# Optimization experiments

Hardware: AMD Instinct MI355X
Metric: run time of the kernel (lower is better)

The kernel has to match this reference:

```python
import jax, jax.numpy as jnp
import numpy as np
import math

B, S, D = 2, 2048, 768
H, KS, VS = 12, 64, 64
MAX_DIST, NUM_BASES, MIN_HALF_LIFE = 1000, 16, 3.0


def _exponential_basis_features():
    # positions -max_dist..max_dist, exponential basis as in RelativePositionalBias
    positions = np.arange(-MAX_DIST, MAX_DIST + 1)
    abs_pos = np.abs(positions).astype(np.float32)
    max_range = math.log2(MAX_DIST)
    half_lives = np.power(2.0, np.linspace(MIN_HALF_LIFE, max_range, NUM_BASES)).reshape(1, -1)
    feats = np.exp(-math.log(2.0) * abs_pos[:, None] / half_lives)  # [2*max_dist+1, num_bases]
    return jnp.asarray(feats, dtype=jnp.float32)


def setup_inputs() -> dict:
    key = jax.random.key(0)
    ks = jax.random.split(key, 6)
    x = jax.random.normal(ks[0], (B, S, D), dtype=jnp.float32)
    # torch nn.Linear weight convention: [out_features, in_features], applied as x @ W.T
    Wq = jax.random.normal(ks[1], (H * KS, D), dtype=jnp.float32) * 0.02
    Wk = jax.random.normal(ks[2], (H * KS, D), dtype=jnp.float32) * 0.02
    Wv = jax.random.normal(ks[3], (H * VS, D), dtype=jnp.float32) * 0.02
    # original zero-inits w_o; use small random for a non-degenerate correctness baseline
    Wo = jax.random.normal(ks[4], (D, H * VS), dtype=jnp.float32) * 0.02
    basis_weights = jax.random.normal(ks[5], (H, NUM_BASES), dtype=jnp.float32)
    basis_features = _exponential_basis_features()  # buffer (non-learned)
    return {"x": x, "Wq": Wq, "Wk": Wk, "Wv": Wv, "Wo": Wo,
            "basis_weights": basis_weights, "basis_features": basis_features}


def _relative_bias(basis_features, basis_weights, q_len, k_len):
    rel = jnp.arange(k_len)[None, :] - jnp.arange(q_len)[:, None]
    rel = jnp.clip(rel, -MAX_DIST, MAX_DIST) + MAX_DIST  # [q, k] indices
    basis = basis_features[rel]                          # [q, k, nb]
    return jnp.einsum('qkb,hb->hqk', basis, basis_weights)


def reference(x, Wq, Wk, Wv, Wo, basis_weights, basis_features):
    b, s, _ = x.shape
    q = (x @ Wq.T).reshape(b, s, H, KS)
    k = (x @ Wk.T).reshape(b, s, H, KS)
    v = (x @ Wv.T).reshape(b, s, H, VS)
    scale = math.sqrt(KS)
    scores = jnp.einsum('bqhc,bkhc->bhqk', q, k) / scale
    scores = scores + _relative_bias(basis_features, basis_weights, s, s)[None]
    attn = jax.nn.softmax(scores, axis=-1)  # dropout is identity in eval
    out = jnp.einsum('bhqk,bkhv->bqhv', attn, v).reshape(b, s, H * VS)
    out = out @ Wo.T
    return out, attn
```

## Files before the change

kernel.cpp:

```cpp
#include <hip/hip_runtime.h>

typedef _Float16 f16;
typedef __attribute__((ext_vector_type(4))) _Float16 f16x4;
typedef __attribute__((ext_vector_type(8))) _Float16 f16x8;
typedef __attribute__((ext_vector_type(4))) float f32x4;
typedef __attribute__((ext_vector_type(16))) float f32x16;

#define B_ 2
#define S_ 2048
#define DMODEL 768
#define H_ 12
#define HS 64
#define NB_ 16
#define QKV_LD 2304

#define ZERO16 {0.f,0.f,0.f,0.f,0.f,0.f,0.f,0.f,0.f,0.f,0.f,0.f,0.f,0.f,0.f,0.f}

__device__ __forceinline__ void gload16(const f16* g, f16* lds) {
    __builtin_amdgcn_global_load_lds((const __attribute__((address_space(1))) void*)g,
                                     (__attribute__((address_space(3))) void*)lds, 16, 0, 0);
}
#define WAIT_VM0_BARRIER()  do { asm volatile("s_waitcnt vmcnt(0) lgkmcnt(0)" ::: "memory"); \
                                 __builtin_amdgcn_s_barrier(); } while (0)

__global__ __launch_bounds__(256) void prep_kernel(const float* __restrict__ x,
                                                   const float* __restrict__ Wq,
                                                   const float* __restrict__ Wk,
                                                   const float* __restrict__ Wv,
                                                   const float* __restrict__ Wo,
                                                   const float* __restrict__ bw,
                                                   const float* __restrict__ bf,
                                                   f16* __restrict__ xb,
                                                   f16* __restrict__ wqkv16,
                                                   f16* __restrict__ wo16,
                                                   float* __restrict__ biasTab) {
    int bid = blockIdx.x;
    int t = threadIdx.x;
    if (bid < 5376) {
        const float* src;
        f16* dst;
        float scale = 1.0f;
        int i;
        if (bid < 3072) {
            i = bid * 256 + t; src = x; dst = xb;
        } else if (bid < 4800) {
            i = (bid - 3072) * 256 + t;
            dst = wqkv16;
            if (i < 147456)      { src = Wq; scale = 0.18033688011112f; }
            else if (i < 294912) { src = Wk - 147456 * 4; }
            else                 { src = Wv - 294912 * 4; }
        } else {
            i = (bid - 4800) * 256 + t; src = Wo; dst = wo16;
        }
        f32x4 v = reinterpret_cast<const f32x4*>(src)[i];
        union { f16 h[4]; unsigned long long u; } o;
        o.h[0] = (f16)(v.x * scale);
        o.h[1] = (f16)(v.y * scale);
        o.h[2] = (f16)(v.z * scale);
        o.h[3] = (f16)(v.w * scale);
        reinterpret_cast<unsigned long long*>(dst)[i] = o.u;
    } else {
        int idx = (bid - 5376) * 256 + t;
        if (idx >= H_ * 4095) return;
        int h = idx / 4095, d = idx % 4095;
        int rel = min(1000, max(-1000, d - 2047));
        int r = rel + 1000;
        float s = 0.f;
#pragma unroll
        for (int tt = 0; tt < NB_; ++tt) s += bf[r * NB_ + tt] * bw[h * NB_ + tt];
        biasTab[h * 4095 + d] = s * 1.44269504088896f;
    }
}

__global__ __launch_bounds__(256) void vtrans_kernel(const f16* __restrict__ qkv,
                                                     f16* __restrict__ vt) {
    __shared__ f16 tile[64][72];
    int blk = blockIdx.x;
    int tb = blk & 31;
    int bh = blk >> 5;
    int b = bh / H_;
    int tok0 = tb << 6;
    int t = threadIdx.x;
    const f16* src = qkv + (size_t)b * S_ * QKV_LD + 1536 + (bh - b * H_) * 64;
#pragma unroll
    for (int j = 0; j < 2; ++j) {
        int u = t + (j << 8);
        int r = u >> 3, c = (u & 7) << 3;
        *reinterpret_cast<f16x8*>(&tile[r][c]) =
            *reinterpret_cast<const f16x8*>(src + (size_t)(tok0 + r) * QKV_LD + c);
    }
    __syncthreads();
    f16* dst = vt + (size_t)bh * 64 * S_ + tok0;
#pragma unroll
    for (int j = 0; j < 2; ++j) {
        int u = t + (j << 8);
        int v = u >> 3, tc = (u & 7) << 3;
        union { f16 h8[8]; f16x8 v8; } o;
#pragma unroll
        for (int i = 0; i < 8; ++i) o.h8[i] = tile[tc + i][v];
        *reinterpret_cast<f16x8*>(&dst[(size_t)v * S_ + tc]) = o.v8;
    }
}

template <typename OutT, int NT>
__global__ __launch_bounds__(256) void gemm_nt(const f16* __restrict__ A,
                                               const f16* __restrict__ Bm,
                                               OutT* __restrict__ C,
                                               int M, int N, int K, float alpha) {
    constexpr int NF  = NT / 32;
    constexpr int BCH = NT / 64;
    __shared__ __align__(16) f16 As[2][128 * 32];
    __shared__ __align__(16) f16 Bs[2][NT * 32];
    const int tiles_n = N / NT;
    int tm = blockIdx.x / tiles_n, tn = blockIdx.x % tiles_n;
    int m0 = tm << 7, n0 = tn * NT;
    int t = threadIdx.x;
    int w = t >> 6, l = t & 63;
    int wr = w >> 1, wc = w & 1;
    int fr = l & 15, hi = l >> 4;
    f32x4 acc[4][NF] = {};

#define GEMM_STAGE(buf, k0)                                                        \
    do {                                                                           \
        _Pragma("unroll")                                                          \
        for (int j = 0; j < 2; ++j) {                                              \
            int u = t + (j << 8);                                                  \
            int row = u >> 2, ch = u & 3;                                          \
            int gcol = (k0) + ((ch ^ (row & 3)) << 3);                             \
            gload16(&A[(size_t)(m0 + row) * K + gcol], As[buf] + (w << 9) + (j << 11)); \
        }                                                                          \
        _Pragma("unroll")                                                          \
        for (int j = 0; j < BCH; ++j) {                                            \
            int u = t + (j << 8);                                                  \
            int row = u >> 2, ch = u & 3;                                          \
            int gcol = (k0) + ((ch ^ (row & 3)) << 3);                             \
            gload16(&Bm[(size_t)(n0 + row) * K + gcol], Bs[buf] + (w << 9) + (j << 11)); \
        }                                                                          \
    } while (0)

    const int nk = K >> 5;
    GEMM_STAGE(0, 0);
    WAIT_VM0_BARRIER();
    for (int kt = 0; kt < nk; ++kt) {
        int buf = kt & 1;
        if (kt + 1 < nk) GEMM_STAGE(buf ^ 1, (kt + 1) << 5);
        f16x8 af[4], bfv[NF];
#pragma unroll
        for (int m = 0; m < 4; ++m) {
            int row = wr * 64 + m * 16 + fr;
            af[m] = *reinterpret_cast<const f16x8*>(&As[buf][row * 32 + ((hi ^ (fr & 3)) << 3)]);
        }
#pragma unroll
        for (int n = 0; n < NF; ++n) {
            int row = wc * (NT / 2) + n * 16 + fr;
            bfv[n] = *reinterpret_cast<const f16x8*>(&Bs[buf][row * 32 + ((hi ^ (fr & 3)) << 3)]);
        }
#pragma unroll
        for (int m = 0; m < 4; ++m)
#pragma unroll
            for (int n = 0; n < NF; ++n)
                acc[m][n] = __builtin_amdgcn_mfma_f32_16x16x32_f16(af[m], bfv[n], acc[m][n], 0, 0, 0);
        WAIT_VM0_BARRIER();
    }
#undef GEMM_STAGE
    int cc = l & 15, cr = (l >> 4) << 2;
#pragma unroll
    for (int m = 0; m < 4; ++m)
#pragma unroll
        for (int n = 0; n < NF; ++n)
#pragma unroll
            for (int j = 0; j < 4; ++j) {
                int rg = m0 + wr * 64 + m * 16 + cr + j;
                int cg = n0 + wc * (NT / 2) + n * 16 + cc;
                C[(size_t)rg * N + cg] = (OutT)(acc[m][n][j] * alpha);
            }
}

#define PSWZ(row) ((((row) >> 2) & 3) << 3)
__global__ __launch_bounds__(256, 3) void attn_kernel(const f16* __restrict__ qp,
                                                      const f16* __restrict__ kp,
                                                      const f16* __restrict__ vt,
                                                      const float* __restrict__ biasTab,
                                                      float* __restrict__ attn_out,
                                                      f16* __restrict__ ctx_out) {
    __shared__ __align__(16) union {
        f16 ks1[2][128 * 64];
        struct { f16 ks[2][64 * 64]; f16 vs[2][64 * 64]; } p2;
    } ar;
    __shared__ __align__(16) f16 psh[64][72];
    __shared__ float bias_l[2112];
    __shared__ float red_l[64][2];
    __shared__ float li_s[64];

    int orig = blockIdx.x;
    int blk = (orig & 7) * 96 + (orig >> 3);
    int qt = blk & 31;
    int bh = blk >> 5;
    int h = bh % H_;
    int b = bh / H_;
    int q0 = qt << 6;

    int t = threadIdx.x;
    int w = t >> 6, l = t & 63;
    int wq = w >> 1, wk = w & 1;
    int col = l & 31;
    int hi = l >> 5;
    int hi4 = hi << 2, hi8 = hi << 3;

    const size_t rowbase = (size_t)b * S_ * QKV_LD + (size_t)h * HS;
    const f16* vbase = vt + (size_t)bh * HS * S_;

    f16x8 qf[4];
    {
        const f16* qrow = qp + rowbase + (size_t)(q0 + wq * 32 + col) * QKV_LD + hi8;
#pragma unroll
        for (int ci = 0; ci < 4; ++ci) qf[ci] = *reinterpret_cast<const f16x8*>(qrow + ci * 16);
    }

    {
        const float* bt = biasTab + h * 4095 + (1984 - q0);
        for (int i = t; i < 2111; i += 256) bias_l[i] = bt[i];
    }

#define P1_STAGE(buf, kb0)                                                          \
    do {                                                                            \
        _Pragma("unroll")                                                           \
        for (int j = 0; j < 4; ++j) {                                               \
            int u = t + (j << 8);                                                   \
            int row = u >> 3, ch = u & 7;                                           \
            gload16(kp + rowbase + (size_t)((kb0) + row) * QKV_LD + ((ch ^ (row & 7)) << 3), \
                    ar.ks1[buf] + (w << 9) + (j << 11));                            \
        }                                                                           \
    } while (0)

    float lsum[16];
#pragma unroll
    for (int r = 0; r < 16; ++r) lsum[r] = 0.f;

    P1_STAGE(0, 0);
    WAIT_VM0_BARRIER();
    for (int jt = 0; jt < 16; ++jt) {
        int buf = jt & 1;
        if (jt + 1 < 16) P1_STAGE(buf ^ 1, (jt + 1) << 7);
#pragma unroll
        for (int half = 0; half < 2; ++half) {
            int krow = half * 64 + wk * 32 + col;
            f32x16 s = ZERO16;
#pragma unroll
            for (int ci = 0; ci < 4; ++ci) {
                f16x8 kf = *reinterpret_cast<const f16x8*>(
                    &ar.ks1[buf][krow * 64 + (((ci * 2 + hi) ^ (krow & 7)) << 3)]);
                s = __builtin_amdgcn_mfma_f32_32x32x16_f16(qf[ci], kf, s, 0, 0, 0);
            }
            int kcol = (jt << 7) + krow;
            const float* bl = bias_l + (kcol + 63 - (wq * 32 + hi4));
#pragma unroll
            for (int r = 0; r < 16; ++r) {
                const int cr = (r & 3) + 8 * (r >> 2);
                lsum[r] += __builtin_amdgcn_exp2f(s[r] + bl[-cr]);
            }
        }
        WAIT_VM0_BARRIER();
    }
#undef P1_STAGE

#pragma unroll
    for (int off = 1; off < 32; off <<= 1) {
#pragma unroll
        for (int r = 0; r < 16; ++r) lsum[r] += __shfl_xor(lsum[r], off);
    }
    if (col == 0) {
#pragma unroll
        for (int r = 0; r < 16; ++r)
            red_l[wq * 32 + (r & 3) + 8 * (r >> 2) + hi4][wk] = lsum[r];
    }
    __syncthreads();
    if (t < 64) li_s[t] = 1.0f / (red_l[t][0] + red_l[t][1]);
    __syncthreads();
    float lreg[16];
#pragma unroll
    for (int r = 0; r < 16; ++r) lreg[r] = li_s[wq * 32 + (r & 3) + 8 * (r >> 2) + hi4];

#define P2_STAGE(buf, kb0)                                                          \
    do {                                                                            \
        _Pragma("unroll")                                                           \
        for (int j = 0; j < 2; ++j) {                                               \
            int u = t + (j << 8);                                                   \
            int row = u >> 3, ch = u & 7;                                           \
            int sw = ((ch ^ (row & 7)) << 3);                                       \
            gload16(kp + rowbase + (size_t)((kb0) + row) * QKV_LD + sw,             \
                    ar.p2.ks[buf] + (w << 9) + (j << 11));                          \
            gload16(vbase + (size_t)row * S_ + (kb0) + sw,                          \
                    ar.p2.vs[buf] + (w << 9) + (j << 11));                          \
        }                                                                           \
    } while (0)

    f32x16 oacc = ZERO16;
    float* aout = attn_out + (((size_t)b * H_ + h) * S_ + q0) * S_;
    const int kcol_loc = wk * 32 + col;

    P2_STAGE(0, 0);
    WAIT_VM0_BARRIER();
    float pstash[16];
    for (int tix = 0; tix < 32; ++tix) {
        int buf = tix & 1;
        int kb0 = tix << 6;
        if (tix + 1 < 32) P2_STAGE(buf ^ 1, kb0 + 64);
        __builtin_amdgcn_sched_barrier(0);
        f32x16 s = ZERO16;
#pragma unroll
        for (int ci = 0; ci < 4; ++ci) {
            f16x8 kf = *reinterpret_cast<const f16x8*>(
                &ar.p2.ks[buf][kcol_loc * 64 + (((ci * 2 + hi) ^ (kcol_loc & 7)) << 3)]);
            s = __builtin_amdgcn_mfma_f32_32x32x16_f16(qf[ci], kf, s, 0, 0, 0);
        }
        int kcol = kb0 + kcol_loc;
        const float* bl = bias_l + (kcol + 63 - (wq * 32 + hi4));
#pragma unroll
        for (int r = 0; r < 16; ++r) {
            const int cr = (r & 3) + 8 * (r >> 2);
            int row = wq * 32 + cr + hi4;
            float p = __builtin_amdgcn_exp2f(s[r] + bl[-cr]) * lreg[r];
            pstash[r] = p;
            psh[row][kcol_loc ^ PSWZ(row)] = (f16)p;
        }
        asm volatile("s_waitcnt lgkmcnt(0)" ::: "memory");
        __builtin_amdgcn_s_barrier();
        __builtin_amdgcn_sched_barrier(0);
        {
            const int rowq = wq * 32 + col;
            const int sw = PSWZ(rowq);
#pragma unroll
            for (int ci = 0; ci < 4; ++ci) {
                f16x8 pa = *reinterpret_cast<const f16x8*>(&psh[rowq][(ci * 16 + hi8) ^ sw]);
                f16x8 vf = *reinterpret_cast<const f16x8*>(
                    &ar.p2.vs[buf][kcol_loc * 64 + (((ci * 2 + hi) ^ (kcol_loc & 7)) << 3)]);
                oacc = __builtin_amdgcn_mfma_f32_32x32x16_f16(pa, vf, oacc, 0, 0, 0);
            }
        }
        asm volatile("s_waitcnt vmcnt(0)" ::: "memory");
        __builtin_amdgcn_s_barrier();
#pragma unroll
        for (int r = 0; r < 16; ++r) {
            const int cr = (r & 3) + 8 * (r >> 2);
            int row = wq * 32 + cr + hi4;
            __builtin_nontemporal_store(pstash[r], &aout[(size_t)row * S_ + kcol]);
        }
    }
#undef P2_STAGE

    {
        f16* cbase = ctx_out + ((size_t)b * S_ + q0) * DMODEL + h * HS + kcol_loc;
#pragma unroll
        for (int r = 0; r < 16; ++r) {
            int row = wq * 32 + (r & 3) + 8 * (r >> 2) + hi4;
            cbase[(size_t)row * DMODEL] = (f16)oacc[r];
        }
    }
}

extern "C" void kernel_launch(void* const* d_in, const int* in_sizes, int n_in,
                              void* d_out, int out_size, void* d_ws, size_t ws_size,
                              hipStream_t stream) {
    const float* x     = (const float*)d_in[0];
    const float* Wq    = (const float*)d_in[1];
    const float* Wk    = (const float*)d_in[2];
    const float* Wv    = (const float*)d_in[3];
    const float* Wo    = (const float*)d_in[4];
    const float* bw    = (const float*)d_in[5];
    const float* bfeat = (const float*)d_in[6];

    char* ws = (char*)d_ws;
    f16*   xb      = (f16*)(ws + 0);
    f16*   vt      = (f16*)(ws + 0);
    f16*   qkv     = (f16*)(ws + 6291456);
    f16*   ctx     = (f16*)(ws + 25165824);
    f16*   wqkv16  = (f16*)(ws + 31457280);
    f16*   wo16    = (f16*)(ws + 34996224);
    float* biasTab = (float*)(ws + 36175872);

    float* out0 = (float*)d_out;
    float* attn = out0 + (size_t)B_ * S_ * DMODEL;

    prep_kernel<<<5568, 256, 0, stream>>>(x, Wq, Wk, Wv, Wo, bw, bfeat,
                                          xb, wqkv16, wo16, biasTab);

    gemm_nt<f16, 128><<<32 * 18, 256, 0, stream>>>(xb, wqkv16, qkv, 4096, QKV_LD, 768, 1.0f);

    vtrans_kernel<<<768, 256, 0, stream>>>(qkv, vt);

    attn_kernel<<<B_ * H_ * (S_ / 64), 256, 0, stream>>>(
        qkv + 0, qkv + 768, vt, biasTab, attn, ctx);

    gemm_nt<float, 64><<<32 * 12, 256, 0, stream>>>(ctx, wo16, out0, 4096, DMODEL, 768, 1.0f);
}
```

Baseline: 171.8 us.

## Split attention into separate row-sum and output kernels for higher occupancy

Splits the fused two-pass attention kernel into two launches. The first kernel computes softmax row sums using 64-row K tiles and smaller LDS, with launch bounds allowing 5 blocks per CU, and writes the inverse sums to workspace. The second kernel reloads Q, bias and the inverse sums, then computes probabilities, the attn output and the context as before. The aim is better latency hiding in the sum pass, at the cost of an extra launch, a second load of Q and bias, and a workspace buffer that reuses the wqkv16 region after the QKV GEMM is done with it.

```diff
diff --git a/kernel.cpp b/kernel.cpp
--- a/kernel.cpp
+++ b/kernel.cpp
@@ -176,21 +176,13 @@
             }
 }
 
-#define PSWZ(row) ((((row) >> 2) & 3) << 3)
-__global__ __launch_bounds__(256, 3) void attn_kernel(const f16* __restrict__ qp,
-                                                      const f16* __restrict__ kp,
-                                                      const f16* __restrict__ vt,
-                                                      const float* __restrict__ biasTab,
-                                                      float* __restrict__ attn_out,
-                                                      f16* __restrict__ ctx_out) {
-    __shared__ __align__(16) union {
-        f16 ks1[2][128 * 64];
-        struct { f16 ks[2][64 * 64]; f16 vs[2][64 * 64]; } p2;
-    } ar;
-    __shared__ __align__(16) f16 psh[64][72];
+__global__ __launch_bounds__(256, 5) void attn_pass1(const f16* __restrict__ qp,
+                                                     const f16* __restrict__ kp,
+                                                     const float* __restrict__ biasTab,
+                                                     float* __restrict__ linv_g) {
+    __shared__ __align__(16) f16 ks[2][64 * 64];
     __shared__ float bias_l[2112];
     __shared__ float red_l[64][2];
-    __shared__ float li_s[64];
 
     int orig = blockIdx.x;
     int blk = (orig & 7) * 96 + (orig >> 3);
@@ -208,7 +200,6 @@
     int hi4 = hi << 2, hi8 = hi << 3;
 
     const size_t rowbase = (size_t)b * S_ * QKV_LD + (size_t)h * HS;
-    const f16* vbase = vt + (size_t)bh * HS * S_;
 
     f16x8 qf[4];
     {
@@ -216,7 +207,6 @@
 #pragma unroll
         for (int ci = 0; ci < 4; ++ci) qf[ci] = *reinterpret_cast<const f16x8*>(qrow + ci * 16);
     }
-
     {
         const float* bt = biasTab + h * 4095 + (1984 - q0);
         for (int i = t; i < 2111; i += 256) bias_l[i] = bt[i];
@@ -225,11 +215,11 @@
 #define P1_STAGE(buf, kb0)                                                          \
     do {                                                                            \
         _Pragma("unroll")                                                           \
-        for (int j = 0; j < 4; ++j) {                                               \
+        for (int j = 0; j < 2; ++j) {                                               \
             int u = t + (j << 8);                                                   \
             int row = u >> 3, ch = u & 7;                                           \
             gload16(kp + rowbase + (size_t)((kb0) + row) * QKV_LD + ((ch ^ (row & 7)) << 3), \
-                    ar.ks1[buf] + (w << 9) + (j << 11));                            \
+                    ks[buf] + (w << 9) + (j << 11));                                \
         }                                                                           \
     } while (0)
 
@@ -239,26 +229,23 @@
 
     P1_STAGE(0, 0);
     WAIT_VM0_BARRIER();
-    for (int jt = 0; jt < 16; ++jt) {
-        int buf = jt & 1;
-        if (jt + 1 < 16) P1_STAGE(buf ^ 1, (jt + 1) << 7);
-#pragma unroll
-        for (int half = 0; half < 2; ++half) {
-            int krow = half * 64 + wk * 32 + col;
-            f32x16 s = ZERO16;
-#pragma unroll
-            for (int ci = 0; ci < 4; ++ci) {
-                f16x8 kf = *reinterpret_cast<const f16x8*>(
-                    &ar.ks1[buf][krow * 64 + (((ci * 2 + hi) ^ (krow & 7)) << 3)]);
-                s = __builtin_amdgcn_mfma_f32_32x32x16_f16(qf[ci], kf, s, 0, 0, 0);
-            }
-            int kcol = (jt << 7) + krow;
-            const float* bl = bias_l + (kcol + 63 - (wq * 32 + hi4));
-#pragma unroll
-            for (int r = 0; r < 16; ++r) {
-                const int cr = (r & 3) + 8 * (r >> 2);
-                lsum[r] += __builtin_amdgcn_exp2f(s[r] + bl[-cr]);
-            }
+    const int krow = wk * 32 + col;
+    for (int tix = 0; tix < 32; ++tix) {
+        int buf = tix & 1;
+        if (tix + 1 < 32) P1_STAGE(buf ^ 1, (tix + 1) << 6);
+        f32x16 s = ZERO16;
+#pragma unroll
+        for (int ci = 0; ci < 4; ++ci) {
+            f16x8 kf = *reinterpret_cast<const f16x8*>(
+                &ks[buf][krow * 64 + (((ci * 2 + hi) ^ (krow & 7)) << 3)]);
+            s = __builtin_amdgcn_mfma_f32_32x32x16_f16(qf[ci], kf, s, 0, 0, 0);
+        }
+        int kcol = (tix << 6) + krow;
+        const float* bl = bias_l + (kcol + 63 - (wq * 32 + hi4));
+#pragma unroll
+        for (int r = 0; r < 16; ++r) {
+            const int cr = (r & 3) + 8 * (r >> 2);
+            lsum[r] += __builtin_amdgcn_exp2f(s[r] + bl[-cr]);
         }
         WAIT_VM0_BARRIER();
     }
@@ -275,11 +262,52 @@
             red_l[wq * 32 + (r & 3) + 8 * (r >> 2) + hi4][wk] = lsum[r];
     }
     __syncthreads();
-    if (t < 64) li_s[t] = 1.0f / (red_l[t][0] + red_l[t][1]);
-    __syncthreads();
-    float lreg[16];
-#pragma unroll
-    for (int r = 0; r < 16; ++r) lreg[r] = li_s[wq * 32 + (r & 3) + 8 * (r >> 2) + hi4];
+    if (t < 64) linv_g[blk * 64 + t] = 1.0f / (red_l[t][0] + red_l[t][1]);
+}
+
+#define PSWZ(row) ((((row) >> 2) & 3) << 3)
+__global__ __launch_bounds__(256, 3) void attn_pass2(const f16* __restrict__ qp,
+                                                     const f16* __restrict__ kp,
+                                                     const f16* __restrict__ vt,
+                                                     const float* __restrict__ biasTab,
+                                                     const float* __restrict__ linv_g,
+                                                     float* __restrict__ attn_out,
+                                                     f16* __restrict__ ctx_out) {
+    __shared__ __align__(16) f16 ks[2][64 * 64];
+    __shared__ __align__(16) f16 vs[2][64 * 64];
+    __shared__ __align__(16) f16 psh[64][72];
+    __shared__ float bias_l[2112];
+    __shared__ float li_s[64];
+
+    int orig = blockIdx.x;
+    int blk = (orig & 7) * 96 + (orig >> 3);
+    int qt = blk & 31;
+    int bh = blk >> 5;
+    int h = bh % H_;
+    int b = bh / H_;
+    int q0 = qt << 6;
+
+    int t = threadIdx.x;
+    int w = t >> 6, l = t & 63;
+    int wq = w >> 1, wk = w & 1;
+    int col = l & 31;
+    int hi = l >> 5;
+    int hi4 = hi << 2, hi8 = hi << 3;
+
+    const size_t rowbase = (size_t)b * S_ * QKV_LD + (size_t)h * HS;
+    const f16* vbase = vt + (size_t)bh * HS * S_;
+
+    f16x8 qf[4];
+    {
+        const f16* qrow = qp + rowbase + (size_t)(q0 + wq * 32 + col) * QKV_LD + hi8;
+#pragma unroll
+        for (int ci = 0; ci < 4; ++ci) qf[ci] = *reinterpret_cast<const f16x8*>(qrow + ci * 16);
+    }
+    {
+        const float* bt = biasTab + h * 4095 + (1984 - q0);
+        for (int i = t; i < 2111; i += 256) bias_l[i] = bt[i];
+    }
+    if (t < 64) li_s[t] = linv_g[blk * 64 + t];
 
 #define P2_STAGE(buf, kb0)                                                          \
     do {                                                                            \
@@ -289,9 +317,9 @@
             int row = u >> 3, ch = u & 7;                                           \
             int sw = ((ch ^ (row & 7)) << 3);                                       \
             gload16(kp + rowbase + (size_t)((kb0) + row) * QKV_LD + sw,             \
-                    ar.p2.ks[buf] + (w << 9) + (j << 11));                          \
+                    ks[buf] + (w << 9) + (j << 11));                                \
             gload16(vbase + (size_t)row * S_ + (kb0) + sw,                          \
-                    ar.p2.vs[buf] + (w << 9) + (j << 11));                          \
+                    vs[buf] + (w << 9) + (j << 11));                                \
         }                                                                           \
     } while (0)
 
@@ -301,6 +329,10 @@
 
     P2_STAGE(0, 0);
     WAIT_VM0_BARRIER();
+    float lreg[16];
+#pragma unroll
+    for (int r = 0; r < 16; ++r) lreg[r] = li_s[wq * 32 + (r & 3) + 8 * (r >> 2) + hi4];
+
     float pstash[16];
     for (int tix = 0; tix < 32; ++tix) {
         int buf = tix & 1;
@@ -311,7 +343,7 @@
 #pragma unroll
         for (int ci = 0; ci < 4; ++ci) {
             f16x8 kf = *reinterpret_cast<const f16x8*>(
-                &ar.p2.ks[buf][kcol_loc * 64 + (((ci * 2 + hi) ^ (kcol_loc & 7)) << 3)]);
+                &ks[buf][kcol_loc * 64 + (((ci * 2 + hi) ^ (kcol_loc & 7)) << 3)]);
             s = __builtin_amdgcn_mfma_f32_32x32x16_f16(qf[ci], kf, s, 0, 0, 0);
         }
         int kcol = kb0 + kcol_loc;
@@ -334,7 +366,7 @@
             for (int ci = 0; ci < 4; ++ci) {
                 f16x8 pa = *reinterpret_cast<const f16x8*>(&psh[rowq][(ci * 16 + hi8) ^ sw]);
                 f16x8 vf = *reinterpret_cast<const f16x8*>(
-                    &ar.p2.vs[buf][kcol_loc * 64 + (((ci * 2 + hi) ^ (kcol_loc & 7)) << 3)]);
+                    &vs[buf][kcol_loc * 64 + (((ci * 2 + hi) ^ (kcol_loc & 7)) << 3)]);
                 oacc = __builtin_amdgcn_mfma_f32_32x32x16_f16(pa, vf, oacc, 0, 0, 0);
             }
         }
@@ -376,6 +408,7 @@
     f16*   qkv     = (f16*)(ws + 6291456);
     f16*   ctx     = (f16*)(ws + 25165824);
     f16*   wqkv16  = (f16*)(ws + 31457280);
+    float* linv    = (float*)(ws + 31457280);
     f16*   wo16    = (f16*)(ws + 34996224);
     float* biasTab = (float*)(ws + 36175872);
 
@@ -389,8 +422,9 @@
 
     vtrans_kernel<<<768, 256, 0, stream>>>(qkv, vt);
 
-    attn_kernel<<<B_ * H_ * (S_ / 64), 256, 0, stream>>>(
-        qkv + 0, qkv + 768, vt, biasTab, attn, ctx);
+    attn_pass1<<<768, 256, 0, stream>>>(qkv + 0, qkv + 768, biasTab, linv);
+
+    attn_pass2<<<768, 256, 0, stream>>>(qkv + 0, qkv + 768, vt, biasTab, linv, attn, ctx);
 
     gemm_nt<float, 64><<<32 * 12, 256, 0, stream>>>(ctx, wo16, out0, 4096, DMODEL, 768, 1.0f);
 }
```

Result: slower. 195.2 us (+13.6%).
